# Kernel optimization log

Hardware: AMD Instinct MI355X
Metric: run time of the kernel (lower is better)

## Reference

```python
import jax, jax.numpy as jnp
import numpy as np

IN_FEATURES = 4096
OUT_FEATURES = 4096
SHARED_ROWS = 512
BATCH = 4096


def setup_inputs() -> dict:
    key = jax.random.key(0)
    k1, k2, k3 = jax.random.split(key, 3)
    x = jax.random.normal(k1, (BATCH, IN_FEATURES), dtype=jnp.float32)
    shared_weights = jax.random.normal(k2, (SHARED_ROWS, IN_FEATURES), dtype=jnp.float32)
    bias = jax.random.normal(k3, (OUT_FEATURES,), dtype=jnp.float32)
    return {"x": x, "shared_weights": shared_weights, "bias": bias}


def reference(x, shared_weights, bias):
    # Original: W = shared_weights.repeat(out_features // shared_rows, 1)  -> [out, in]
    #           y = x @ W.T + bias
    # Row i of W equals shared_weights[i % shared_rows], so the output columns are a
    # tile of the small GEMM result — compute the small GEMM once and tile (same math,
    # avoids materializing the full [out, in] weight).
    reps = OUT_FEATURES // SHARED_ROWS
    y_small = jnp.einsum("bi,ri->br", x, shared_weights)  # [batch, shared_rows]
    y = jnp.tile(y_small, (1, reps)) + bias  # [batch, out_features]
    return y
```

## Files before the change

### kernel.cpp

```cpp
#include <hip/hip_runtime.h>
#include <hip/hip_bf16.h>


typedef __bf16 bf8 __attribute__((ext_vector_type(8)));
typedef float f4 __attribute__((ext_vector_type(4)));
typedef unsigned int uint;
typedef unsigned short ushort;

constexpr int M = 4096;
constexpr int K = 4096;
constexpr int NS = 512;
constexpr int OUTF = 4096;
constexpr int BM = 64, BN = 64, BK = 64;
constexpr int NITER = K / BK;
constexpr int SSTR = 68;

#define PERM_HI2(hi, lo) __builtin_amdgcn_perm((hi), (lo), 0x07060302u)
#define WAITCNT_VM4 0xF74
#define WAITCNT_VM0 0xF70

__device__ __forceinline__ void async16(const ushort* g, ushort* l) {
  __builtin_amdgcn_global_load_lds(
      (const __attribute__((address_space(1))) void*)g,
      (__attribute__((address_space(3))) void*)l, 16, 0, 0);
}

__global__ __launch_bounds__(256)
void convert_kernel(const float* __restrict__ x, const float* __restrict__ w,
                    ushort* __restrict__ xb, ushort* __restrict__ wb) {
  const size_t i = (size_t)blockIdx.x * 256 + threadIdx.x;
  constexpr size_t NX = (size_t)M * K / 8;
  const float* src;
  ushort* dst;
  if (i < NX) { src = x + i * 8; dst = xb + i * 8; }
  else        { const size_t j = i - NX; src = w + j * 8; dst = wb + j * 8; }
  const uint4 a = *reinterpret_cast<const uint4*>(src);
  const uint4 b = *reinterpret_cast<const uint4*>(src + 4);
  uint4 o;
  o.x = PERM_HI2(a.y, a.x); o.y = PERM_HI2(a.w, a.z);
  o.z = PERM_HI2(b.y, b.x); o.w = PERM_HI2(b.w, b.z);
  *reinterpret_cast<uint4*>(dst) = o;
}

__global__ __launch_bounds__(256, 2)
void gemm_kernel(const ushort* __restrict__ xb, const ushort* __restrict__ wb,
                 const float* __restrict__ bias, float* __restrict__ out) {
  __shared__ __align__(16) ushort As[3][BM * BK];
  __shared__ __align__(16) ushort Bs[3][BN * BK];

  const int b  = blockIdx.x;
  const int mt = ((b >> 6) << 3) | (b & 7);
  const int nt = (b >> 3) & 7;

  const int tid  = threadIdx.x;
  const int wv   = tid >> 6;
  const int lane = tid & 63;

  int goff[2], lloc[2];
#pragma unroll
  for (int j = 0; j < 2; ++j) {
    const int c = (wv * 2 + j) * 64 + lane;
    const int r = c >> 3;
    const int g = (c & 7) ^ (r & 7);
    goff[j] = r * K + g * 8;
    lloc[j] = (wv * 2 + j) * 512;
  }

  const ushort* xT = xb + (size_t)(mt * BM) * K;
  const ushort* wT = wb + (size_t)(nt * BN) * K;

  const int wm = (wv & 1) * 32;
  const int wn = (wv >> 1) * 32;
  const int lr = lane & 15;
  const int lq = lane >> 4;

  f4 acc[2][2] = {};

  auto issue = [&](int tile, int stage) {
    const int ko = tile * BK;
#pragma unroll
    for (int j = 0; j < 2; ++j) {
      async16(xT + ko + goff[j], &As[stage][lloc[j]]);
      async16(wT + ko + goff[j], &Bs[stage][lloc[j]]);
    }
  };

  issue(0, 0);
  issue(1, 1);

  int st = 0;
  for (int kk = 0; kk < NITER; ++kk) {
    if (kk + 1 < NITER) __builtin_amdgcn_s_waitcnt(WAITCNT_VM4);
    else                __builtin_amdgcn_s_waitcnt(WAITCNT_VM0);
    __builtin_amdgcn_s_barrier();
    asm volatile("" ::: "memory");

    if (kk + 2 < NITER) {
      int st2 = st + 2; if (st2 >= 3) st2 -= 3;
      issue(kk + 2, st2);
    }

    const ushort* aT = As[st];
    const ushort* bT = Bs[st];
#pragma unroll
    for (int t = 0; t < 2; ++t) {
      const int sc = ((t * 4 + lq) ^ (lr & 7)) * 8;
      bf8 af[2], bfv[2];
#pragma unroll
      for (int mf = 0; mf < 2; ++mf)
        af[mf] = *reinterpret_cast<const bf8*>(&aT[(wm + mf * 16 + lr) * BK + sc]);
#pragma unroll
      for (int nf = 0; nf < 2; ++nf)
        bfv[nf] = *reinterpret_cast<const bf8*>(&bT[(wn + nf * 16 + lr) * BK + sc]);
#pragma unroll
      for (int mf = 0; mf < 2; ++mf)
#pragma unroll
        for (int nf = 0; nf < 2; ++nf)
          acc[mf][nf] = __builtin_amdgcn_mfma_f32_16x16x32_bf16(af[mf], bfv[nf], acc[mf][nf], 0, 0, 0);
    }
    asm volatile("" ::: "memory");

    if (++st >= 3) st = 0;
  }

  __syncthreads();
  float* sc = reinterpret_cast<float*>(&As[0][0]);
#pragma unroll
  for (int mf = 0; mf < 2; ++mf)
#pragma unroll
    for (int nf = 0; nf < 2; ++nf)
#pragma unroll
      for (int r = 0; r < 4; ++r)
        sc[(wm + mf * 16 + lq * 4 + r) * SSTR + wn + nf * 16 + lr] = acc[mf][nf][r];
  __syncthreads();

  const int c4 = tid & 15;
  const int r0 = (tid >> 4) * 4;
  const float4* bias4 = reinterpret_cast<const float4*>(bias);
  float4 bb[8];
#pragma unroll
  for (int rep = 0; rep < 8; ++rep)
    bb[rep] = bias4[rep * 128 + nt * 16 + c4];

#pragma unroll
  for (int rr = 0; rr < 4; ++rr) {
    const int row = r0 + rr;
    const float4 v = *reinterpret_cast<const float4*>(&sc[row * SSTR + c4 * 4]);
    float* orow = out + (size_t)(mt * BM + row) * OUTF + nt * BN + c4 * 4;
#pragma unroll
    for (int rep = 0; rep < 8; ++rep) {
      float4 o;
      o.x = v.x + bb[rep].x; o.y = v.y + bb[rep].y;
      o.z = v.z + bb[rep].z; o.w = v.w + bb[rep].w;
      *reinterpret_cast<float4*>(orow + rep * NS) = o;
    }
  }
}

extern "C" void kernel_launch(void* const* d_in, const int* in_sizes, int n_in,
                              void* d_out, int out_size, void* d_ws, size_t ws_size,
                              hipStream_t stream) {
  (void)in_sizes; (void)n_in; (void)out_size; (void)ws_size;
  const float* x    = (const float*)d_in[0];
  const float* w    = (const float*)d_in[1];
  const float* bias = (const float*)d_in[2];
  float* out = (float*)d_out;

  ushort* xb = (ushort*)d_ws;
  ushort* wb = (ushort*)d_ws + (size_t)M * K;

  constexpr int conv_blocks = (int)(((size_t)M * K / 8 + (size_t)NS * K / 8) / 256);
  convert_kernel<<<dim3(conv_blocks), dim3(256), 0, stream>>>(x, w, xb, wb);
  gemm_kernel<<<dim3(64 * 8), dim3(256), 0, stream>>>(xb, wb, bias, out);
}
```

Before: 162.7 us.

## Use 128x128 tiles with 4-way split-K and ticket-based reduction in output

Doubles the block tile to 128x128 (4x4 MFMA fragments per wave) and splits K four ways so the grid stays at 512 blocks. Each split writes its fp32 partial into an otherwise-unused tile column slot of the output, then bumps an atomic ticket. The last-arriving block sums the four partials, adds bias, and writes all eight replicated column tiles. Staging drops from a 3-stage to a 2-stage buffer with an extra barrier per iteration. The aim is more operand reuse per block, at the cost of extra global traffic for partials and the ordering risks of the ticket scheme.

```diff
diff --git a/kernel.cpp b/kernel.cpp
--- a/kernel.cpp
+++ b/kernel.cpp
@@ -11,12 +11,17 @@
 constexpr int K = 4096;
 constexpr int NS = 512;
 constexpr int OUTF = 4096;
-constexpr int BM = 64, BN = 64, BK = 64;
-constexpr int NITER = K / BK;
-constexpr int SSTR = 68;
+
+constexpr int BM = 128, BN = 128, BK = 64;
+constexpr int SPLITS = 4;
+constexpr int KSPL = K / SPLITS;
+constexpr int NITER = KSPL / BK;
+constexpr int MT = M / BM;
+constexpr int NT = NS / BN;
+constexpr int NTILES = MT * NT;
 
 #define PERM_HI2(hi, lo) __builtin_amdgcn_perm((hi), (lo), 0x07060302u)
-#define WAITCNT_VM4 0xF74
+#define WAITCNT_VM8 0xF78
 #define WAITCNT_VM0 0xF70
 
 __device__ __forceinline__ void async16(const ushort* g, ushort* l) {
@@ -27,7 +32,9 @@
 
 __global__ __launch_bounds__(256)
 void convert_kernel(const float* __restrict__ x, const float* __restrict__ w,
-                    ushort* __restrict__ xb, ushort* __restrict__ wb) {
+                    ushort* __restrict__ xb, ushort* __restrict__ wb,
+                    uint* __restrict__ tickets) {
+  if (blockIdx.x == 0 && threadIdx.x < NTILES) tickets[threadIdx.x] = 0u;
   const size_t i = (size_t)blockIdx.x * 256 + threadIdx.x;
   constexpr size_t NX = (size_t)M * K / 8;
   const float* src;
@@ -35,124 +42,142 @@
   if (i < NX) { src = x + i * 8; dst = xb + i * 8; }
   else        { const size_t j = i - NX; src = w + j * 8; dst = wb + j * 8; }
   const uint4 a = *reinterpret_cast<const uint4*>(src);
-  const uint4 b = *reinterpret_cast<const uint4*>(src + 4);
+  const uint4 bq = *reinterpret_cast<const uint4*>(src + 4);
   uint4 o;
-  o.x = PERM_HI2(a.y, a.x); o.y = PERM_HI2(a.w, a.z);
-  o.z = PERM_HI2(b.y, b.x); o.w = PERM_HI2(b.w, b.z);
+  o.x = PERM_HI2(a.y, a.x);  o.y = PERM_HI2(a.w, a.z);
+  o.z = PERM_HI2(bq.y, bq.x); o.w = PERM_HI2(bq.w, bq.z);
   *reinterpret_cast<uint4*>(dst) = o;
 }
 
 __global__ __launch_bounds__(256, 2)
 void gemm_kernel(const ushort* __restrict__ xb, const ushort* __restrict__ wb,
-                 const float* __restrict__ bias, float* __restrict__ out) {
-  __shared__ __align__(16) ushort As[3][BM * BK];
-  __shared__ __align__(16) ushort Bs[3][BN * BK];
-
-  const int b  = blockIdx.x;
-  const int mt = ((b >> 6) << 3) | (b & 7);
-  const int nt = (b >> 3) & 7;
-
+                 const float* __restrict__ bias, float* __restrict__ out,
+                 uint* __restrict__ tickets) {
+  __shared__ __align__(16) ushort As[2][BM * BK];
+  __shared__ __align__(16) ushort Bs[2][BN * BK];
+
+  const int b    = blockIdx.x;
+  const int xcd  = b & 7;
+  const int slot = b >> 3;
+  const int nt   = slot & 3;
+  const int g    = (slot >> 2) * 8 + xcd;
+  const int mt   = g >> 2;
+  const int ks   = g & 2 ? (g & 3) : (g & 3);
   const int tid  = threadIdx.x;
   const int wv   = tid >> 6;
   const int lane = tid & 63;
 
-  int goff[2], lloc[2];
-#pragma unroll
-  for (int j = 0; j < 2; ++j) {
-    const int c = (wv * 2 + j) * 64 + lane;
-    const int r = c >> 3;
-    const int g = (c & 7) ^ (r & 7);
-    goff[j] = r * K + g * 8;
-    lloc[j] = (wv * 2 + j) * 512;
-  }
-
-  const ushort* xT = xb + (size_t)(mt * BM) * K;
-  const ushort* wT = wb + (size_t)(nt * BN) * K;
-
-  const int wm = (wv & 1) * 32;
-  const int wn = (wv >> 1) * 32;
+  int goff[4], lloc[4];
+#pragma unroll
+  for (int j = 0; j < 4; ++j) {
+    const int c  = (wv * 4 + j) * 64 + lane;
+    const int r  = c >> 3;
+    const int gs = (c & 7) ^ (r & 7);
+    goff[j] = r * K + gs * 8;
+    lloc[j] = (wv * 4 + j) * 512;
+  }
+
+  const ushort* xT = xb + (size_t)(mt * BM) * K + ks * KSPL;
+  const ushort* wT = wb + (size_t)(nt * BN) * K + ks * KSPL;
+
+  auto issue = [&](int tile, int stg) {
+    const int ko = tile * BK;
+#pragma unroll
+    for (int j = 0; j < 4; ++j) async16(xT + ko + goff[j], &As[stg][lloc[j]]);
+#pragma unroll
+    for (int j = 0; j < 4; ++j) async16(wT + ko + goff[j], &Bs[stg][lloc[j]]);
+  };
+
+  const int wm = (wv & 1) * 64;
+  const int wn = (wv >> 1) * 64;
   const int lr = lane & 15;
   const int lq = lane >> 4;
 
-  f4 acc[2][2] = {};
-
-  auto issue = [&](int tile, int stage) {
-    const int ko = tile * BK;
-#pragma unroll
-    for (int j = 0; j < 2; ++j) {
-      async16(xT + ko + goff[j], &As[stage][lloc[j]]);
-      async16(wT + ko + goff[j], &Bs[stage][lloc[j]]);
-    }
-  };
+  f4 acc[4][4] = {};
 
   issue(0, 0);
   issue(1, 1);
 
   int st = 0;
   for (int kk = 0; kk < NITER; ++kk) {
-    if (kk + 1 < NITER) __builtin_amdgcn_s_waitcnt(WAITCNT_VM4);
+    if (kk + 1 < NITER) __builtin_amdgcn_s_waitcnt(WAITCNT_VM8);
     else                __builtin_amdgcn_s_waitcnt(WAITCNT_VM0);
     __builtin_amdgcn_s_barrier();
     asm volatile("" ::: "memory");
 
-    if (kk + 2 < NITER) {
-      int st2 = st + 2; if (st2 >= 3) st2 -= 3;
-      issue(kk + 2, st2);
-    }
-
     const ushort* aT = As[st];
     const ushort* bT = Bs[st];
 #pragma unroll
     for (int t = 0; t < 2; ++t) {
       const int sc = ((t * 4 + lq) ^ (lr & 7)) * 8;
-      bf8 af[2], bfv[2];
-#pragma unroll
-      for (int mf = 0; mf < 2; ++mf)
+      bf8 af[4], bfv[4];
+#pragma unroll
+      for (int mf = 0; mf < 4; ++mf)
         af[mf] = *reinterpret_cast<const bf8*>(&aT[(wm + mf * 16 + lr) * BK + sc]);
 #pragma unroll
-      for (int nf = 0; nf < 2; ++nf)
+      for (int nf = 0; nf < 4; ++nf)
         bfv[nf] = *reinterpret_cast<const bf8*>(&bT[(wn + nf * 16 + lr) * BK + sc]);
 #pragma unroll
-      for (int mf = 0; mf < 2; ++mf)
-#pragma unroll
-        for (int nf = 0; nf < 2; ++nf)
+      for (int mf = 0; mf < 4; ++mf)
+#pragma unroll
+        for (int nf = 0; nf < 4; ++nf)
           acc[mf][nf] = __builtin_amdgcn_mfma_f32_16x16x32_bf16(af[mf], bfv[nf], acc[mf][nf], 0, 0, 0);
     }
     asm volatile("" ::: "memory");
-
-    if (++st >= 3) st = 0;
-  }
+    __builtin_amdgcn_s_barrier();
+    asm volatile("" ::: "memory");
+    if (kk + 2 < NITER) issue(kk + 2, st);
+    st ^= 1;
+  }
+
+  float* pbase = out + (size_t)(mt * BM) * OUTF + nt * BN + ks * NS;
+#pragma unroll
+  for (int mf = 0; mf < 4; ++mf)
+#pragma unroll
+    for (int nf = 0; nf < 4; ++nf)
+#pragma unroll
+      for (int r = 0; r < 4; ++r)
+        pbase[(size_t)(wm + mf * 16 + lq * 4 + r) * OUTF + wn + nf * 16 + lr] =
+            acc[mf][nf][r];
 
   __syncthreads();
-  float* sc = reinterpret_cast<float*>(&As[0][0]);
-#pragma unroll
-  for (int mf = 0; mf < 2; ++mf)
-#pragma unroll
-    for (int nf = 0; nf < 2; ++nf)
-#pragma unroll
-      for (int r = 0; r < 4; ++r)
-        sc[(wm + mf * 16 + lq * 4 + r) * SSTR + wn + nf * 16 + lr] = acc[mf][nf][r];
+  uint* s_oldp = reinterpret_cast<uint*>(&As[0][0]);
+  if (tid == 0) {
+    __threadfence();
+    *s_oldp = __hip_atomic_fetch_add(&tickets[mt * NT + nt], 1u,
+                                     __ATOMIC_ACQ_REL, __HIP_MEMORY_SCOPE_AGENT);
+  }
   __syncthreads();
-
-  const int c4 = tid & 15;
-  const int r0 = (tid >> 4) * 4;
+  if (*s_oldp != SPLITS - 1) return;
+
+  if (tid == 0) __threadfence();
+  __syncthreads();
+
+  const int c4 = tid & 31;
+  const int rg = tid >> 5;
   const float4* bias4 = reinterpret_cast<const float4*>(bias);
   float4 bb[8];
 #pragma unroll
   for (int rep = 0; rep < 8; ++rep)
-    bb[rep] = bias4[rep * 128 + nt * 16 + c4];
-
-#pragma unroll
-  for (int rr = 0; rr < 4; ++rr) {
-    const int row = r0 + rr;
-    const float4 v = *reinterpret_cast<const float4*>(&sc[row * SSTR + c4 * 4]);
-    float* orow = out + (size_t)(mt * BM + row) * OUTF + nt * BN + c4 * 4;
+    bb[rep] = bias4[rep * 128 + nt * 32 + c4];
+
+  float* obase = out + (size_t)(mt * BM) * OUTF + nt * BN;
+#pragma unroll 4
+  for (int rr = 0; rr < 16; ++rr) {
+    const int row = rg + rr * 8;
+    float* orow = obase + (size_t)row * OUTF;
+    float sx = 0.f, sy = 0.f, sz = 0.f, sw = 0.f;
+#pragma unroll
+    for (int sp = 0; sp < SPLITS; ++sp) {
+      const float4 p = *reinterpret_cast<const float4*>(orow + sp * NS + c4 * 4);
+      sx += p.x; sy += p.y; sz += p.z; sw += p.w;
+    }
 #pragma unroll
     for (int rep = 0; rep < 8; ++rep) {
       float4 o;
-      o.x = v.x + bb[rep].x; o.y = v.y + bb[rep].y;
-      o.z = v.z + bb[rep].z; o.w = v.w + bb[rep].w;
-      *reinterpret_cast<float4*>(orow + rep * NS) = o;
+      o.x = sx + bb[rep].x; o.y = sy + bb[rep].y;
+      o.z = sz + bb[rep].z; o.w = sw + bb[rep].w;
+      *reinterpret_cast<float4*>(orow + rep * NS + c4 * 4) = o;
     }
   }
 }
@@ -167,9 +192,10 @@
   float* out = (float*)d_out;
 
   ushort* xb = (ushort*)d_ws;
-  ushort* wb = (ushort*)d_ws + (size_t)M * K;
+  ushort* wb = xb + (size_t)M * K;
+  uint* tickets = (uint*)(wb + (size_t)NS * K);
 
   constexpr int conv_blocks = (int)(((size_t)M * K / 8 + (size_t)NS * K / 8) / 256);
-  convert_kernel<<<dim3(conv_blocks), dim3(256), 0, stream>>>(x, w, xb, wb);
-  gemm_kernel<<<dim3(64 * 8), dim3(256), 0, stream>>>(xb, wb, bias, out);
-}
+  convert_kernel<<<dim3(conv_blocks), dim3(256), 0, stream>>>(x, w, xb, wb, tickets);
+  gemm_kernel<<<dim3(MT * NT * SPLITS), dim3(256), 0, stream>>>(xb, wb, bias, out, tickets);
+}
```

Measured after the change: 236.7 us. 45.5% more time.

## Fuse x fp32-to-bf16 conversion into GEMM tile loads

Applied to the files above, without the earlier changes.

Drops the standalone conversion pass over x. The GEMM now streams fp32 x tiles straight into LDS with a new swizzle and truncates them to bf16 in registers before the MFMA. This avoids writing and rereading a 32 MB bf16 copy of x. In exchange, LDS use per block rises (the fp32 A tiles are twice as large, which may cut occupancy below 2 blocks per CU), each x tile is fetched in fp32 by all 8 column-tile blocks, and more permute work sits in the inner loop.

```diff
diff --git a/kernel.cpp b/kernel.cpp
--- a/kernel.cpp
+++ b/kernel.cpp
@@ -16,24 +16,20 @@
 constexpr int SSTR = 68;
 
 #define PERM_HI2(hi, lo) __builtin_amdgcn_perm((hi), (lo), 0x07060302u)
-#define WAITCNT_VM4 0xF74
+#define WAITCNT_VM6 0xF76
 #define WAITCNT_VM0 0xF70
 
-__device__ __forceinline__ void async16(const ushort* g, ushort* l) {
+__device__ __forceinline__ void async16(const void* g, void* l) {
   __builtin_amdgcn_global_load_lds(
       (const __attribute__((address_space(1))) void*)g,
       (__attribute__((address_space(3))) void*)l, 16, 0, 0);
 }
 
 __global__ __launch_bounds__(256)
-void convert_kernel(const float* __restrict__ x, const float* __restrict__ w,
-                    ushort* __restrict__ xb, ushort* __restrict__ wb) {
+void convert_w(const float* __restrict__ w, ushort* __restrict__ wb) {
   const size_t i = (size_t)blockIdx.x * 256 + threadIdx.x;
-  constexpr size_t NX = (size_t)M * K / 8;
-  const float* src;
-  ushort* dst;
-  if (i < NX) { src = x + i * 8; dst = xb + i * 8; }
-  else        { const size_t j = i - NX; src = w + j * 8; dst = wb + j * 8; }
+  const float* src = w + i * 8;
+  ushort* dst = wb + i * 8;
   const uint4 a = *reinterpret_cast<const uint4*>(src);
   const uint4 b = *reinterpret_cast<const uint4*>(src + 4);
   uint4 o;
@@ -43,9 +39,9 @@
 }
 
 __global__ __launch_bounds__(256, 2)
-void gemm_kernel(const ushort* __restrict__ xb, const ushort* __restrict__ wb,
+void gemm_kernel(const float* __restrict__ x, const ushort* __restrict__ wb,
                  const float* __restrict__ bias, float* __restrict__ out) {
-  __shared__ __align__(16) ushort As[3][BM * BK];
+  __shared__ __align__(16) float  As[3][BM * BK];
   __shared__ __align__(16) ushort Bs[3][BN * BK];
 
   const int b  = blockIdx.x;
@@ -56,17 +52,26 @@
   const int wv   = tid >> 6;
   const int lane = tid & 63;
 
-  int goff[2], lloc[2];
+  int goffA[4], llocA[4];
+#pragma unroll
+  for (int j = 0; j < 4; ++j) {
+    const int c = (wv * 4 + j) * 64 + lane;
+    const int r = c >> 4;
+    const int g = (c & 15) ^ (r & 15);
+    goffA[j] = r * K + g * 4;
+    llocA[j] = (wv * 4 + j) * 256;
+  }
+  int goffB[2], llocB[2];
 #pragma unroll
   for (int j = 0; j < 2; ++j) {
     const int c = (wv * 2 + j) * 64 + lane;
     const int r = c >> 3;
     const int g = (c & 7) ^ (r & 7);
-    goff[j] = r * K + g * 8;
-    lloc[j] = (wv * 2 + j) * 512;
+    goffB[j] = r * K + g * 8;
+    llocB[j] = (wv * 2 + j) * 512;
   }
 
-  const ushort* xT = xb + (size_t)(mt * BM) * K;
+  const float*  xT = x  + (size_t)(mt * BM) * K;
   const ushort* wT = wb + (size_t)(nt * BN) * K;
 
   const int wm = (wv & 1) * 32;
@@ -79,10 +84,11 @@
   auto issue = [&](int tile, int stage) {
     const int ko = tile * BK;
 #pragma unroll
-    for (int j = 0; j < 2; ++j) {
-      async16(xT + ko + goff[j], &As[stage][lloc[j]]);
-      async16(wT + ko + goff[j], &Bs[stage][lloc[j]]);
-    }
+    for (int j = 0; j < 4; ++j)
+      async16(xT + ko + goffA[j], &As[stage][llocA[j]]);
+#pragma unroll
+    for (int j = 0; j < 2; ++j)
+      async16(wT + ko + goffB[j], &Bs[stage][llocB[j]]);
   };
 
   issue(0, 0);
@@ -90,7 +96,7 @@
 
   int st = 0;
   for (int kk = 0; kk < NITER; ++kk) {
-    if (kk + 1 < NITER) __builtin_amdgcn_s_waitcnt(WAITCNT_VM4);
+    if (kk + 1 < NITER) __builtin_amdgcn_s_waitcnt(WAITCNT_VM6);
     else                __builtin_amdgcn_s_waitcnt(WAITCNT_VM0);
     __builtin_amdgcn_s_barrier();
     asm volatile("" ::: "memory");
@@ -100,15 +106,25 @@
       issue(kk + 2, st2);
     }
 
-    const ushort* aT = As[st];
+    const float*  aT = As[st];
     const ushort* bT = Bs[st];
 #pragma unroll
     for (int t = 0; t < 2; ++t) {
-      const int sc = ((t * 4 + lq) ^ (lr & 7)) * 8;
       bf8 af[2], bfv[2];
 #pragma unroll
-      for (int mf = 0; mf < 2; ++mf)
-        af[mf] = *reinterpret_cast<const bf8*>(&aT[(wm + mf * 16 + lr) * BK + sc]);
+      for (int mf = 0; mf < 2; ++mf) {
+        const int row = wm + mf * 16 + lr;
+        const int ca  = ((t * 4 + lq) * 2) ^ lr;
+        const f4 a0 = *reinterpret_cast<const f4*>(&aT[row * BK + ca * 4]);
+        const f4 a1 = *reinterpret_cast<const f4*>(&aT[row * BK + (ca ^ 1) * 4]);
+        const uint* u0 = reinterpret_cast<const uint*>(&a0);
+        const uint* u1 = reinterpret_cast<const uint*>(&a1);
+        uint4 p;
+        p.x = PERM_HI2(u0[1], u0[0]); p.y = PERM_HI2(u0[3], u0[2]);
+        p.z = PERM_HI2(u1[1], u1[0]); p.w = PERM_HI2(u1[3], u1[2]);
+        af[mf] = __builtin_bit_cast(bf8, p);
+      }
+      const int sc = ((t * 4 + lq) ^ (lr & 7)) * 8;
 #pragma unroll
       for (int nf = 0; nf < 2; ++nf)
         bfv[nf] = *reinterpret_cast<const bf8*>(&bT[(wn + nf * 16 + lr) * BK + sc]);
@@ -124,14 +140,14 @@
   }
 
   __syncthreads();
-  float* sc = reinterpret_cast<float*>(&As[0][0]);
+  float* scr = &As[0][0];
 #pragma unroll
   for (int mf = 0; mf < 2; ++mf)
 #pragma unroll
     for (int nf = 0; nf < 2; ++nf)
 #pragma unroll
       for (int r = 0; r < 4; ++r)
-        sc[(wm + mf * 16 + lq * 4 + r) * SSTR + wn + nf * 16 + lr] = acc[mf][nf][r];
+        scr[(wm + mf * 16 + lq * 4 + r) * SSTR + wn + nf * 16 + lr] = acc[mf][nf][r];
   __syncthreads();
 
   const int c4 = tid & 15;
@@ -145,7 +161,7 @@
 #pragma unroll
   for (int rr = 0; rr < 4; ++rr) {
     const int row = r0 + rr;
-    const float4 v = *reinterpret_cast<const float4*>(&sc[row * SSTR + c4 * 4]);
+    const float4 v = *reinterpret_cast<const float4*>(&scr[row * SSTR + c4 * 4]);
     float* orow = out + (size_t)(mt * BM + row) * OUTF + nt * BN + c4 * 4;
 #pragma unroll
     for (int rep = 0; rep < 8; ++rep) {
@@ -166,10 +182,9 @@
   const float* bias = (const float*)d_in[2];
   float* out = (float*)d_out;
 
-  ushort* xb = (ushort*)d_ws;
-  ushort* wb = (ushort*)d_ws + (size_t)M * K;
+  ushort* wb = (ushort*)d_ws;
 
-  constexpr int conv_blocks = (int)(((size_t)M * K / 8 + (size_t)NS * K / 8) / 256);
-  convert_kernel<<<dim3(conv_blocks), dim3(256), 0, stream>>>(x, w, xb, wb);
-  gemm_kernel<<<dim3(64 * 8), dim3(256), 0, stream>>>(xb, wb, bias, out);
+  constexpr int convw_blocks = (int)((size_t)NS * K / 8 / 256);
+  convert_w<<<dim3(convw_blocks), dim3(256), 0, stream>>>(w, wb);
+  gemm_kernel<<<dim3(64 * 8), dim3(256), 0, stream>>>(x, wb, bias, out);
 }
```

Measured after the change: 174.9 us. 1.08x slower.

## Use 32x32x16 MFMA with split-K across waves and LDS reduction

Applied to the files above, without the earlier changes.

Each wave now computes the full 64x64 tile with four 32x32x16 bf16 MFMAs over its own 16-wide slice of the K=64 chunk, instead of a 32x32 quadrant built from 16x16x32 MFMAs. Partial sums from the four waves are reduced through LDS in the epilogue, in four row-quarters with barriers, before bias add and tiled stores. The aim is fewer LDS fragment loads per MFMA and the higher throughput of the larger MFMA shape. In exchange the epilogue needs a cross-wave reduction and extra synchronisation, and each lane holds more accumulator registers.

```diff
diff --git a/kernel.cpp b/kernel.cpp
--- a/kernel.cpp
+++ b/kernel.cpp
@@ -3,7 +3,7 @@
 
 
 typedef __bf16 bf8 __attribute__((ext_vector_type(8)));
-typedef float f4 __attribute__((ext_vector_type(4)));
+typedef float f16v __attribute__((ext_vector_type(16)));
 typedef unsigned int uint;
 typedef unsigned short ushort;
 
@@ -14,6 +14,7 @@
 constexpr int BM = 64, BN = 64, BK = 64;
 constexpr int NITER = K / BK;
 constexpr int SSTR = 68;
+constexpr int WSTR = 16 * SSTR;
 
 #define PERM_HI2(hi, lo) __builtin_amdgcn_perm((hi), (lo), 0x07060302u)
 #define WAITCNT_VM4 0xF74
@@ -69,13 +70,6 @@
   const ushort* xT = xb + (size_t)(mt * BM) * K;
   const ushort* wT = wb + (size_t)(nt * BN) * K;
 
-  const int wm = (wv & 1) * 32;
-  const int wn = (wv >> 1) * 32;
-  const int lr = lane & 15;
-  const int lq = lane >> 4;
-
-  f4 acc[2][2] = {};
-
   auto issue = [&](int tile, int stage) {
     const int ko = tile * BK;
 #pragma unroll
@@ -84,6 +78,12 @@
       async16(wT + ko + goff[j], &Bs[stage][lloc[j]]);
     }
   };
+
+  const int l31 = lane & 31;
+  const int hi  = lane >> 5;
+  const int coff = ((2 * wv + hi) ^ (lane & 7)) * 8;
+
+  f16v acc[2][2] = {};
 
   issue(0, 0);
   issue(1, 1);
@@ -102,40 +102,24 @@
 
     const ushort* aT = As[st];
     const ushort* bT = Bs[st];
-#pragma unroll
-    for (int t = 0; t < 2; ++t) {
-      const int sc = ((t * 4 + lq) ^ (lr & 7)) * 8;
-      bf8 af[2], bfv[2];
-#pragma unroll
-      for (int mf = 0; mf < 2; ++mf)
-        af[mf] = *reinterpret_cast<const bf8*>(&aT[(wm + mf * 16 + lr) * BK + sc]);
-#pragma unroll
-      for (int nf = 0; nf < 2; ++nf)
-        bfv[nf] = *reinterpret_cast<const bf8*>(&bT[(wn + nf * 16 + lr) * BK + sc]);
-#pragma unroll
-      for (int mf = 0; mf < 2; ++mf)
-#pragma unroll
-        for (int nf = 0; nf < 2; ++nf)
-          acc[mf][nf] = __builtin_amdgcn_mfma_f32_16x16x32_bf16(af[mf], bfv[nf], acc[mf][nf], 0, 0, 0);
-    }
+    const bf8 a0 = *reinterpret_cast<const bf8*>(&aT[(l31)      * BK + coff]);
+    const bf8 a1 = *reinterpret_cast<const bf8*>(&aT[(32 + l31) * BK + coff]);
+    const bf8 b0 = *reinterpret_cast<const bf8*>(&bT[(l31)      * BK + coff]);
+    const bf8 b1 = *reinterpret_cast<const bf8*>(&bT[(32 + l31) * BK + coff]);
+    acc[0][0] = __builtin_amdgcn_mfma_f32_32x32x16_bf16(a0, b0, acc[0][0], 0, 0, 0);
+    acc[0][1] = __builtin_amdgcn_mfma_f32_32x32x16_bf16(a0, b1, acc[0][1], 0, 0, 0);
+    acc[1][0] = __builtin_amdgcn_mfma_f32_32x32x16_bf16(a1, b0, acc[1][0], 0, 0, 0);
+    acc[1][1] = __builtin_amdgcn_mfma_f32_32x32x16_bf16(a1, b1, acc[1][1], 0, 0, 0);
     asm volatile("" ::: "memory");
 
     if (++st >= 3) st = 0;
   }
 
   __syncthreads();
-  float* sc = reinterpret_cast<float*>(&As[0][0]);
-#pragma unroll
-  for (int mf = 0; mf < 2; ++mf)
-#pragma unroll
-    for (int nf = 0; nf < 2; ++nf)
-#pragma unroll
-      for (int r = 0; r < 4; ++r)
-        sc[(wm + mf * 16 + lq * 4 + r) * SSTR + wn + nf * 16 + lr] = acc[mf][nf][r];
-  __syncthreads();
+  float* scr = reinterpret_cast<float*>(&As[0][0]);
 
-  const int c4 = tid & 15;
-  const int r0 = (tid >> 4) * 4;
+  const int c4  = tid & 15;
+  const int r16 = tid >> 4;
   const float4* bias4 = reinterpret_cast<const float4*>(bias);
   float4 bb[8];
 #pragma unroll
@@ -143,17 +127,36 @@
     bb[rep] = bias4[rep * 128 + nt * 16 + c4];
 
 #pragma unroll
-  for (int rr = 0; rr < 4; ++rr) {
-    const int row = r0 + rr;
-    const float4 v = *reinterpret_cast<const float4*>(&sc[row * SSTR + c4 * 4]);
-    float* orow = out + (size_t)(mt * BM + row) * OUTF + nt * BN + c4 * 4;
+  for (int rq = 0; rq < 4; ++rq) {
+    const int tm = rq >> 1, half = rq & 1;
+#pragma unroll
+    for (int tn = 0; tn < 2; ++tn)
+#pragma unroll
+      for (int j = 0; j < 8; ++j) {
+        const int row16 = (j & 3) + 8 * (j >> 2) + 4 * hi;
+        scr[wv * WSTR + row16 * SSTR + tn * 32 + l31] = acc[tm][tn][8 * half + j];
+      }
+    __syncthreads();
+    float4 s;
+    {
+      const float4 p0 = *reinterpret_cast<const float4*>(&scr[0 * WSTR + r16 * SSTR + c4 * 4]);
+      const float4 p1 = *reinterpret_cast<const float4*>(&scr[1 * WSTR + r16 * SSTR + c4 * 4]);
+      const float4 p2 = *reinterpret_cast<const float4*>(&scr[2 * WSTR + r16 * SSTR + c4 * 4]);
+      const float4 p3 = *reinterpret_cast<const float4*>(&scr[3 * WSTR + r16 * SSTR + c4 * 4]);
+      s.x = (p0.x + p1.x) + (p2.x + p3.x);
+      s.y = (p0.y + p1.y) + (p2.y + p3.y);
+      s.z = (p0.z + p1.z) + (p2.z + p3.z);
+      s.w = (p0.w + p1.w) + (p2.w + p3.w);
+    }
+    float* orow = out + (size_t)(mt * BM + rq * 16 + r16) * OUTF + nt * BN + c4 * 4;
 #pragma unroll
     for (int rep = 0; rep < 8; ++rep) {
       float4 o;
-      o.x = v.x + bb[rep].x; o.y = v.y + bb[rep].y;
-      o.z = v.z + bb[rep].z; o.w = v.w + bb[rep].w;
+      o.x = s.x + bb[rep].x; o.y = s.y + bb[rep].y;
+      o.z = s.z + bb[rep].z; o.w = s.w + bb[rep].w;
       *reinterpret_cast<float4*>(orow + rep * NS) = o;
     }
+    __syncthreads();
   }
 }
 
```

Result: no change. 161.6 us (-0.6%).
